# Kernel tuning notes

Measured on AMD Instinct MI355X. Metric: run time of the kernel, lower is better.

## Reference

```python
import jax, jax.numpy as jnp
import numpy as np

C = 1.0            # curvature
KEEP_RATIO = 0.5
MIN_NORM = 1e-15
BALL_EPS = 4e-3    # hgcn PoincareBall projection epsilon


def _norm(x):
    return jnp.maximum(jnp.linalg.norm(x, axis=-1, keepdims=True), MIN_NORM)


def proj(x, c):
    n = _norm(x)
    maxnorm = (1.0 - BALL_EPS) / jnp.sqrt(c)
    return jnp.where(n > maxnorm, x / n * maxnorm, x)


def expmap0(u, c):
    sc = jnp.sqrt(c)
    n = _norm(u)
    return jnp.tanh(sc * n) * u / (sc * n)


def logmap0(p, c):
    # proj_tan0 is identity on the Poincare ball
    sc = jnp.sqrt(c)
    n = _norm(p)
    t = jnp.clip(sc * n, -1.0 + 1e-7, 1.0 - 1e-7)
    return jnp.arctanh(t) * p / (sc * n)


def mobius_add(x, y, c):
    x2 = jnp.sum(x * x, -1, keepdims=True)
    y2 = jnp.sum(y * y, -1, keepdims=True)
    xy = jnp.sum(x * y, -1, keepdims=True)
    num = (1 + 2 * c * xy + c * y2) * x + (1 - c * x2) * y
    den = 1 + 2 * c * xy + c * c * x2 * y2
    return num / jnp.maximum(den, MIN_NORM)


def setup_inputs() -> dict:
    key = jax.random.key(0)
    N, D, E = 100000, 512, 3200000
    k0, k1, k2, k3, k4 = jax.random.split(key, 5)
    # points must lie inside the Poincare ball: scale down then project
    x = 0.01 * jax.random.normal(k0, (N, D), jnp.float32)
    x = proj(x, C)
    weight = jax.random.normal(k1, (D, 1), jnp.float32) * float(np.sqrt(6.0 / (D + 1)))  # xavier-ish
    bias = jnp.zeros((1,), jnp.float32)
    adj_vals = jax.random.uniform(k2, (E,), jnp.float32)
    edge_rows = jax.random.randint(k3, (E,), 0, N, jnp.int32)
    edge_cols = jax.random.randint(k4, (E,), 0, N, jnp.int32)
    return {
        "input_feature": x,
        "adj_vals": adj_vals,
        "weight": weight,
        "bias": bias,
        "w1": jnp.float32(0.5),
        "b": jnp.float32(0.0),
        "edge_rows": edge_rows,
        "edge_cols": edge_cols,
    }


def reference(input_feature, adj_vals, weight, bias, w1, b, edge_rows, edge_cols):
    N = input_feature.shape[0]
    # --- HypGraphConvolution(input_dim -> 1) ---
    x_tan = logmap0(input_feature, C)              # [N, D]
    support = x_tan @ weight                       # [N, 1]
    hyp_bias = proj(expmap0(bias[None, :], C), C)  # [1, 1]
    support = proj(mobius_add(support, hyp_bias, C), C)
    # sparse adj @ support via gather + segment_sum
    gathered = adj_vals[:, None] * support[edge_cols]            # [E, 1]
    agg = jax.ops.segment_sum(gathered, edge_rows, num_segments=N)  # [N, 1]
    score = proj(expmap0(agg, C), C)
    # --- pooling head ---
    attn = jnp.tanh(score[:, 0])                   # squeeze -> [N]
    norm = jnp.sqrt(C) * jnp.linalg.norm(input_feature, axis=-1)  # manifold.normalize
    attn = w1 * attn + (1 - w1) * (1 - norm) + b
    k = int(KEEP_RATIO * N)
    _, idx = jax.lax.top_k(attn, k)
    idx = jnp.sort(idx)                            # boolean mask preserves node order
    x_euc = logmap0(input_feature, C)              # logmap0 then proj_tan0 (identity)
    hidden = x_euc[idx] * attn[idx][:, None]       # [k, D]
    return hidden, attn
```

## Files before the change

kernel.cpp:

```cpp
#include <hip/hip_runtime.h>
#include <stdint.h>

#define CHUNK 3072
#define BROWS 256

__global__ __launch_bounds__(256) void rowstats(
    const float* __restrict__ x, const float* __restrict__ w,
    const float* __restrict__ bias, const float* __restrict__ w1p,
    const float* __restrict__ bp,
    float* __restrict__ support, float* __restrict__ coef,
    double* __restrict__ base, int N)
{
    int wv = threadIdx.x >> 6, lane = threadIdx.x & 63;
    int row = blockIdx.x * 4 + wv;
    if (row >= N) return;
    const float4* xr = (const float4*)(x + (size_t)row * 512);
    const float4* wr = (const float4*)(w);
    float dot = 0.f, ss = 0.f;
#pragma unroll
    for (int it = 0; it < 2; it++) {
        float4 xv = xr[lane + it * 64];
        float4 wv4 = wr[lane + it * 64];
        dot += xv.x * wv4.x + xv.y * wv4.y + xv.z * wv4.z + xv.w * wv4.w;
        ss  += xv.x * xv.x + xv.y * xv.y + xv.z * xv.z + xv.w * xv.w;
    }
    for (int off = 32; off; off >>= 1) {
        dot += __shfl_xor(dot, off);
        ss  += __shfl_xor(ss, off);
    }
    if (lane == 0) {
        double n = sqrt((double)ss); if (n < 1e-15) n = 1e-15;
        double t = n; const double lim = 1.0 - 1e-7; if (t > lim) t = lim;
        double cf = atanh(t) / n;
        double s = cf * (double)dot;
        double b0 = (double)bias[0];
        double nb = fabs(b0); if (nb < 1e-15) nb = 1e-15;
        double hb = tanh(nb) * b0 / nb;
        const double maxn = 0.996;
        double nh = fabs(hb); if (nh < 1e-15) nh = 1e-15;
        if (nh > maxn) hb = hb / nh * maxn;
        double x2 = s * s, y2 = hb * hb, xy = s * hb;
        double num = (1.0 + 2.0 * xy + y2) * s + (1.0 - x2) * hb;
        double den = 1.0 + 2.0 * xy + x2 * y2;
        if (den < 1e-15) den = 1e-15;
        double r = num / den;
        double nr = fabs(r); if (nr < 1e-15) nr = 1e-15;
        if (nr > maxn) r = r / nr * maxn;
        support[row] = (float)r;
        coef[row] = (float)cf;
        double w1 = (double)w1p[0];
        double bb = (double)bp[0];
        base[row] = (1.0 - w1) * (1.0 - n) + bb;
    }
}

__global__ __launch_bounds__(256) void spmv(
    const int* __restrict__ rows, const int* __restrict__ cols,
    const float* __restrict__ adj, const float* __restrict__ support,
    unsigned long long* __restrict__ agg, int E)
{
    int e = blockIdx.x * 256 + threadIdx.x;
    if (e >= E) return;
    double p = (double)adj[e] * (double)support[cols[e]];
    long long f = llrint(p * 1073741824.0);
    atomicAdd(&agg[rows[e]], (unsigned long long)f);
}

__global__ __launch_bounds__(256) void edge_hist(
    const int* __restrict__ rows, uint32_t* __restrict__ P,
    int E, int nbuk, int nchunks)
{
    __shared__ uint32_t h[512];
    int b = blockIdx.x;
    for (int q = threadIdx.x; q < 512; q += 256) h[q] = 0u;
    __syncthreads();
    int s = b * CHUNK, e_end = min(E, s + CHUNK);
    for (int i = s + threadIdx.x; i < e_end; i += 256)
        atomicAdd(&h[((uint32_t)rows[i]) >> 8], 1u);
    __syncthreads();
    for (int q = threadIdx.x; q < nbuk; q += 256)
        P[(size_t)q * nchunks + b] = h[q];
}

__global__ __launch_bounds__(64) void scan_parts(
    uint32_t* __restrict__ P, uint32_t* __restrict__ tot, int nchunks)
{
    int q = blockIdx.x, lane = threadIdx.x;
    uint32_t* row = P + (size_t)q * nchunks;
    uint32_t run = 0;
    for (int base = 0; base < nchunks; base += 64) {
        int idx = base + lane;
        uint32_t v = (idx < nchunks) ? row[idx] : 0u;
        uint32_t inc = v;
        for (int off = 1; off < 64; off <<= 1) {
            uint32_t t = __shfl_up(inc, off);
            if (lane >= off) inc += t;
        }
        if (idx < nchunks) row[idx] = run + inc - v;
        run += __shfl(inc, 63);
    }
    if (lane == 0) tot[q] = run;
}

__global__ __launch_bounds__(1024) void scan_base(
    const uint32_t* __restrict__ tot, uint32_t* __restrict__ bas, int nbuk)
{
    __shared__ uint32_t lds[1024];
    int t = threadIdx.x;
    uint32_t v = (t < nbuk) ? tot[t] : 0u;
    lds[t] = v;
    __syncthreads();
    for (int off = 1; off < 1024; off <<= 1) {
        uint32_t u = (t >= off) ? lds[t - off] : 0u;
        __syncthreads();
        lds[t] += u;
        __syncthreads();
    }
    if (t == 0) bas[0] = 0u;
    if (t < nbuk) bas[t + 1] = lds[t];
}

__global__ __launch_bounds__(256) void edge_sort_scatter(
    const int* __restrict__ rows, const int* __restrict__ cols,
    const float* __restrict__ adj, const float* __restrict__ support,
    const uint32_t* __restrict__ P, const uint32_t* __restrict__ bas,
    int* __restrict__ prod, uint8_t* __restrict__ rowlo,
    int E, int nbuk, int nchunks)
{
    __shared__ uint32_t lcnt[512], lofs[512], gbase[512], sc[512];
    __shared__ int      lpi[CHUNK];
    __shared__ uint16_t lq[CHUNK];
    __shared__ uint8_t  lrl[CHUNK];
    int b = blockIdx.x, t = threadIdx.x;
    int s = b * CHUNK;
    int n = min(CHUNK, E - s);
    if (n <= 0) return;
    for (int q = t; q < 512; q += 256) lcnt[q] = 0u;
    __syncthreads();
    for (int i = t; i < n; i += 256)
        atomicAdd(&lcnt[((uint32_t)rows[s + i]) >> 8], 1u);
    __syncthreads();
    uint32_t a0 = lcnt[t], a1 = lcnt[t + 256];
    sc[t] = a0; sc[t + 256] = a1;
    __syncthreads();
    for (int off = 1; off < 512; off <<= 1) {
        uint32_t u0 = (t >= off) ? sc[t - off] : 0u;
        uint32_t u1 = ((t + 256) >= off) ? sc[t + 256 - off] : 0u;
        __syncthreads();
        sc[t] += u0; sc[t + 256] += u1;
        __syncthreads();
    }
    lofs[t] = sc[t] - a0;
    lofs[t + 256] = sc[t + 256] - a1;
    for (int q = t; q < 512; q += 256) {
        gbase[q] = (q < nbuk) ? (bas[q] + P[(size_t)q * nchunks + b]) : 0u;
        lcnt[q] = 0u;
    }
    __syncthreads();
    for (int i = t; i < n; i += 256) {
        uint32_t r = (uint32_t)rows[s + i];
        uint32_t q = r >> 8;
        double p = (double)adj[s + i] * (double)support[cols[s + i]];
        int pi = (int)llrint(p * 1073741824.0);
        uint32_t rank = atomicAdd(&lcnt[q], 1u);
        uint32_t slot = lofs[q] + rank;
        lpi[slot] = pi;
        lq[slot]  = (uint16_t)q;
        lrl[slot] = (uint8_t)(r & 255u);
    }
    __syncthreads();
    for (int i = t; i < n; i += 256) {
        uint32_t q = lq[i];
        uint32_t gpos = gbase[q] + ((uint32_t)i - lofs[q]);
        prod[gpos]  = lpi[i];
        rowlo[gpos] = lrl[i];
    }
}

__global__ __launch_bounds__(256) void bucket_reduce(
    const int* __restrict__ prod, const uint8_t* __restrict__ rowlo,
    const uint32_t* __restrict__ bas, unsigned long long* __restrict__ agg, int N)
{
    __shared__ unsigned long long acc[BROWS];
    int q = blockIdx.x;
    acc[threadIdx.x] = 0ull;
    __syncthreads();
    uint32_t s = bas[q], e = bas[q + 1];
    for (uint32_t i = s + threadIdx.x; i < e; i += 256)
        atomicAdd(&acc[rowlo[i]], (unsigned long long)(long long)prod[i]);
    __syncthreads();
    int gr = q * BROWS + threadIdx.x;
    if (gr < N) agg[gr] = acc[threadIdx.x];
}

__global__ __launch_bounds__(256) void attn_kernel(
    const unsigned long long* __restrict__ agg, const double* __restrict__ base,
    const float* __restrict__ w1p,
    float* __restrict__ attn, uint32_t* __restrict__ keys,
    uint32_t* __restrict__ hist1, float* __restrict__ attn_out, int N)
{
    int i = blockIdx.x * 256 + threadIdx.x;
    if (i >= N) return;
    double a = (double)(long long)agg[i] * (1.0 / 1073741824.0);
    double na = fabs(a); if (na < 1e-15) na = 1e-15;
    double sc_ = tanh(na) * a / na;
    const double maxn = 0.996;
    double ns = fabs(sc_); if (ns < 1e-15) ns = 1e-15;
    if (ns > maxn) sc_ = sc_ / ns * maxn;
    double w1 = (double)w1p[0];
    double at = w1 * tanh(sc_) + base[i];
    float af = (float)at;
    attn[i] = af;
    attn_out[i] = af;
    union { float f; uint32_t u; } cv; cv.f = af;
    uint32_t key = cv.u ^ ((cv.u >> 31) ? 0xFFFFFFFFu : 0x80000000u);
    keys[i] = key;
    atomicAdd(&hist1[key >> 16], 1u);
}

__global__ __launch_bounds__(1024) void select_bucket(
    const uint32_t* __restrict__ hist, uint32_t* M, int mode, uint32_t k)
{
    __shared__ uint32_t lds[1024];
    int t = threadIdx.x;
    uint32_t ktarget = (mode == 0) ? k : (k - M[1]);
    uint32_t csum = 0;
    for (int j = 0; j < 64; j++) csum += hist[t * 64 + j];
    lds[t] = csum;
    __syncthreads();
    for (int off = 1; off < 1024; off <<= 1) {
        uint32_t v = (t + off < 1024) ? lds[t + off] : 0u;
        __syncthreads();
        lds[t] += v;
        __syncthreads();
    }
    uint32_t run = (t + 1 < 1024) ? lds[t + 1] : 0u;
    for (int j = 63; j >= 0; j--) {
        uint32_t c = hist[t * 64 + j];
        uint32_t nr = run + c;
        if (nr >= ktarget && run < ktarget) {
            if (mode == 0) { M[0] = (uint32_t)(t * 64 + j); M[1] = run; }
            else           { M[2] = (M[0] << 16) | (uint32_t)(t * 64 + j); }
        }
        run = nr;
    }
}

__global__ __launch_bounds__(256) void hist_low(
    const uint32_t* __restrict__ keys, const uint32_t* __restrict__ M,
    uint32_t* __restrict__ hist2, int N)
{
    int i = blockIdx.x * 256 + threadIdx.x;
    if (i >= N) return;
    uint32_t key = keys[i];
    if ((key >> 16) == M[0]) atomicAdd(&hist2[key & 0xFFFFu], 1u);
}

__global__ __launch_bounds__(256) void blocksum(
    const uint32_t* __restrict__ keys, const uint32_t* __restrict__ M,
    uint32_t* __restrict__ bs, uint32_t* __restrict__ bt, int N)
{
    __shared__ uint32_t ls[4], lt[4];
    uint32_t tau = M[2];
    int base_i = blockIdx.x * 1024 + threadIdx.x * 4;
    uint32_t cs = 0, ct = 0;
    for (int j = 0; j < 4; j++) {
        int i = base_i + j;
        if (i < N) {
            uint32_t kk = keys[i];
            cs += (kk > tau);
            ct += (kk == tau);
        }
    }
    for (int off = 32; off; off >>= 1) {
        cs += __shfl_xor(cs, off);
        ct += __shfl_xor(ct, off);
    }
    int lane = threadIdx.x & 63, wv = threadIdx.x >> 6;
    if (lane == 0) { ls[wv] = cs; lt[wv] = ct; }
    __syncthreads();
    if (threadIdx.x == 0) {
        uint32_t a = 0, b = 0;
        for (int wq = 0; wq < 4; wq++) { a += ls[wq]; b += lt[wq]; }
        bs[blockIdx.x] = a; bt[blockIdx.x] = b;
    }
}

__global__ __launch_bounds__(128) void scanblocks(
    uint32_t* M, const uint32_t* __restrict__ bsv, const uint32_t* __restrict__ btv,
    uint32_t* __restrict__ ssv, uint32_t* __restrict__ stv, int nb, uint32_t k)
{
    __shared__ uint32_t A[128], B[128];
    int t = threadIdx.x;
    if (nb <= 128) {
        uint32_t a = (t < nb) ? bsv[t] : 0u;
        uint32_t b = (t < nb) ? btv[t] : 0u;
        A[t] = a; B[t] = b;
        __syncthreads();
        for (int off = 1; off < 128; off <<= 1) {
            uint32_t ua = (t >= off) ? A[t - off] : 0u;
            uint32_t ub = (t >= off) ? B[t - off] : 0u;
            __syncthreads();
            A[t] += ua; B[t] += ub;
            __syncthreads();
        }
        if (t < nb) { ssv[t] = A[t] - a; stv[t] = B[t] - b; }
        if (t == 127) M[3] = k - A[127];
    } else if (t == 0) {
        uint32_t a = 0, b = 0;
        for (int i = 0; i < nb; i++) {
            ssv[i] = a; stv[i] = b;
            a += bsv[i]; b += btv[i];
        }
        M[3] = k - a;
    }
}

__global__ __launch_bounds__(256) void select_write(
    const uint32_t* __restrict__ keys, const uint32_t* __restrict__ M,
    const uint32_t* __restrict__ ss, const uint32_t* __restrict__ st,
    uint32_t* __restrict__ sel, int N)
{
    uint32_t tau = M[2], need = M[3];
    int t = threadIdx.x, lane = t & 63, wv = t >> 6;
    int base_i = blockIdx.x * 1024 + t * 4;
    uint32_t fs[4], ft[4];
    uint32_t cs = 0, ct = 0;
    for (int j = 0; j < 4; j++) {
        int i = base_i + j;
        uint32_t kk = (i < N) ? keys[i] : 0u;
        fs[j] = (i < N) && (kk > tau);
        ft[j] = (i < N) && (kk == tau);
        cs += fs[j]; ct += ft[j];
    }
    uint32_t is_ = cs, it_ = ct;
    for (int off = 1; off < 64; off <<= 1) {
        uint32_t vs = __shfl_up(is_, off);
        uint32_t vt = __shfl_up(it_, off);
        if (lane >= off) { is_ += vs; it_ += vt; }
    }
    uint32_t wes = is_ - cs, wet = it_ - ct;
    __shared__ uint32_t lws[4], lwt[4];
    if (lane == 63) { lws[wv] = is_; lwt[wv] = it_; }
    __syncthreads();
    uint32_t wos = 0, wot = 0;
    for (int wq = 0; wq < wv; wq++) { wos += lws[wq]; wot += lwt[wq]; }
    uint32_t gs = ss[blockIdx.x] + wos + wes;
    uint32_t gt = st[blockIdx.x] + wot + wet;
    for (int j = 0; j < 4; j++) {
        int i = base_i + j;
        if (fs[j]) {
            uint32_t pos = gs + (gt < need ? gt : need);
            sel[pos] = (uint32_t)i;
        } else if (ft[j]) {
            if (gt < need) sel[gs + gt] = (uint32_t)i;
        }
        gs += fs[j]; gt += ft[j];
    }
}

__global__ __launch_bounds__(256) void write_hidden(
    const float* __restrict__ x, const uint32_t* __restrict__ sel,
    const float* __restrict__ attn, const float* __restrict__ coef,
    float* __restrict__ out, int K)
{
    int wv = threadIdx.x >> 6, lane = threadIdx.x & 63;
    int p = blockIdx.x * 4 + wv;
    if (p >= K) return;
    uint32_t i = sel[p];
    float s = attn[i] * coef[i];
    const float4* xr = (const float4*)(x + (size_t)i * 512);
    float4* orow = (float4*)(out + (size_t)p * 512);
#pragma unroll
    for (int it = 0; it < 2; it++) {
        float4 v = xr[lane + it * 64];
        float4 o;
        o.x = v.x * s; o.y = v.y * s; o.z = v.z * s; o.w = v.w * s;
        orow[lane + it * 64] = o;
    }
}

extern "C" void kernel_launch(void* const* d_in, const int* in_sizes, int n_in,
                              void* d_out, int out_size, void* d_ws, size_t ws_size,
                              hipStream_t stream)
{
    const float* x    = (const float*)d_in[0];
    const float* adj  = (const float*)d_in[1];
    const float* w    = (const float*)d_in[2];
    const float* bias = (const float*)d_in[3];
    const float* w1p  = (const float*)d_in[4];
    const float* bp   = (const float*)d_in[5];
    const int* erow = (const int*)d_in[6];
    const int* ecol = (const int*)d_in[7];

    int D = in_sizes[2];
    int N = in_sizes[0] / D;
    int E = in_sizes[1];
    int K = N / 2;

    char* ws = (char*)d_ws;
    float*   support = (float*)(ws);
    float*   coef    = (float*)(ws + (512 << 10));
    double*  base    = (double*)(ws + (1 << 20));
    float*   attn    = (float*)(ws + (2 << 20));
    uint32_t* keys   = (uint32_t*)(ws + (2 << 20) + (512 << 10));
    unsigned long long* agg = (unsigned long long*)(ws + (3 << 20));
    uint32_t* hist1  = (uint32_t*)(ws + (4 << 20));
    uint32_t* hist2  = (uint32_t*)(ws + (4 << 20) + (256 << 10));
    uint32_t* M      = (uint32_t*)(ws + 4718592);
    uint32_t* bsv = M + 8;
    uint32_t* btv = M + 8 + 128;
    uint32_t* ssv = M + 8 + 256;
    uint32_t* stv = M + 8 + 384;
    uint32_t* sel  = (uint32_t*)(ws + 4849664);
    uint32_t* tot  = (uint32_t*)(ws + 5242880);
    uint32_t* bas  = (uint32_t*)(ws + 5242880 + 4096);
    uint32_t* P    = (uint32_t*)(ws + 5242880 + 16384);
    int*      prod = (int*)(ws + (9 << 20));
    uint8_t*  rowlo= (uint8_t*)(ws + (22 << 20));

    float* hidden_out = (float*)d_out;
    float* attn_out   = (float*)d_out + (size_t)K * D;

    int nbuk = (N + BROWS - 1) / BROWS;
    int nchunks = (E + CHUNK - 1) / CHUNK;
    bool fast = (ws_size >= (size_t)(26 << 20)) && (nbuk <= 512) &&
                ((size_t)nbuk * nchunks * 4 <= (size_t)(3 << 20) + (1008 << 10));

    hipMemsetAsync(ws + (4 << 20), 0, (512 << 10) + 4096, stream);

    rowstats<<<(N + 3) / 4, 256, 0, stream>>>(x, w, bias, w1p, bp, support, coef, base, N);

    if (fast) {
        edge_hist<<<nchunks, 256, 0, stream>>>(erow, P, E, nbuk, nchunks);
        scan_parts<<<nbuk, 64, 0, stream>>>(P, tot, nchunks);
        scan_base<<<1, 1024, 0, stream>>>(tot, bas, nbuk);
        edge_sort_scatter<<<nchunks, 256, 0, stream>>>(erow, ecol, adj, support, P, bas,
                                                       prod, rowlo, E, nbuk, nchunks);
        bucket_reduce<<<nbuk, 256, 0, stream>>>(prod, rowlo, bas, agg, N);
    } else {
        hipMemsetAsync(agg, 0, (size_t)N * 8, stream);
        spmv<<<(E + 255) / 256, 256, 0, stream>>>(erow, ecol, adj, support, agg, E);
    }

    attn_kernel<<<(N + 255) / 256, 256, 0, stream>>>(agg, base, w1p, attn, keys, hist1, attn_out, N);
    select_bucket<<<1, 1024, 0, stream>>>(hist1, M, 0, (uint32_t)K);
    hist_low<<<(N + 255) / 256, 256, 0, stream>>>(keys, M, hist2, N);
    select_bucket<<<1, 1024, 0, stream>>>(hist2, M, 1, (uint32_t)K);
    int nb = (N + 1023) / 1024;
    blocksum<<<nb, 256, 0, stream>>>(keys, M, bsv, btv, N);
    scanblocks<<<1, 128, 0, stream>>>(M, bsv, btv, ssv, stv, nb, (uint32_t)K);
    select_write<<<nb, 256, 0, stream>>>(keys, M, ssv, stv, sel, N);
    write_hidden<<<(K + 3) / 4, 256, 0, stream>>>(x, sel, attn, coef, hidden_out, K);
}
```

Baseline: 409.8 us.

## Cut kernel launches: fixed-capacity buckets, fused reduce+attn, single-block radix select

Each row bucket now gets a fixed slot of CAP entries, which removes the global base scan kernel. Bucket reduction is fused with the attention/key/histogram computation, and the memset is folded into rowstats. The multi-kernel radix top-k (select_bucket, hist_low, blocksum, scanblocks, select_write) is replaced by one single-block find_tau and a select_write2 that recomputes prefix counts by scanning all earlier keys. The aim is to cut launch and sync overhead, in exchange for silently dropping edges if a bucket exceeds CAP, quadratic key rescanning in select_write2, and a single-block serial pass over N keys. A branch also skips the Möbius add when the bias is zero.

```diff
diff --git a/kernel.cpp b/kernel.cpp
--- a/kernel.cpp
+++ b/kernel.cpp
@@ -3,14 +3,19 @@
 
 #define CHUNK 3072
 #define BROWS 256
+#define CAP   12288
 
 __global__ __launch_bounds__(256) void rowstats(
     const float* __restrict__ x, const float* __restrict__ w,
     const float* __restrict__ bias, const float* __restrict__ w1p,
     const float* __restrict__ bp,
     float* __restrict__ support, float* __restrict__ coef,
-    double* __restrict__ base, int N)
-{
+    double* __restrict__ base,
+    uint32_t* __restrict__ hist1, uint32_t* __restrict__ M, int N)
+{
+    if (blockIdx.x < 256) hist1[blockIdx.x * 256 + threadIdx.x] = 0u;
+    else if (blockIdx.x == 256 && threadIdx.x < 8) M[threadIdx.x] = 0u;
+
     int wv = threadIdx.x >> 6, lane = threadIdx.x & 63;
     int row = blockIdx.x * 4 + wv;
     if (row >= N) return;
@@ -33,17 +38,22 @@
         double t = n; const double lim = 1.0 - 1e-7; if (t > lim) t = lim;
         double cf = atanh(t) / n;
         double s = cf * (double)dot;
+        const double maxn = 0.996;
         double b0 = (double)bias[0];
-        double nb = fabs(b0); if (nb < 1e-15) nb = 1e-15;
-        double hb = tanh(nb) * b0 / nb;
-        const double maxn = 0.996;
-        double nh = fabs(hb); if (nh < 1e-15) nh = 1e-15;
-        if (nh > maxn) hb = hb / nh * maxn;
-        double x2 = s * s, y2 = hb * hb, xy = s * hb;
-        double num = (1.0 + 2.0 * xy + y2) * s + (1.0 - x2) * hb;
-        double den = 1.0 + 2.0 * xy + x2 * y2;
-        if (den < 1e-15) den = 1e-15;
-        double r = num / den;
+        double r;
+        if (b0 == 0.0) {
+            r = s;
+        } else {
+            double nb = fabs(b0); if (nb < 1e-15) nb = 1e-15;
+            double hb = tanh(nb) * b0 / nb;
+            double nh = fabs(hb); if (nh < 1e-15) nh = 1e-15;
+            if (nh > maxn) hb = hb / nh * maxn;
+            double x2 = s * s, y2 = hb * hb, xy = s * hb;
+            double num = (1.0 + 2.0 * xy + y2) * s + (1.0 - x2) * hb;
+            double den = 1.0 + 2.0 * xy + x2 * y2;
+            if (den < 1e-15) den = 1e-15;
+            r = num / den;
+        }
         double nr = fabs(r); if (nr < 1e-15) nr = 1e-15;
         if (nr > maxn) r = r / nr * maxn;
         support[row] = (float)r;
@@ -54,6 +64,16 @@
     }
 }
 
+__device__ __forceinline__ float attn_math(double a, double base_i, double w1)
+{
+    double na = fabs(a); if (na < 1e-15) na = 1e-15;
+    double sc_ = tanh(na) * a / na;
+    const double maxn = 0.996;
+    double ns = fabs(sc_); if (ns < 1e-15) ns = 1e-15;
+    if (ns > maxn) sc_ = sc_ / ns * maxn;
+    return (float)(w1 * tanh(sc_) + base_i);
+}
+
 __global__ __launch_bounds__(256) void spmv(
     const int* __restrict__ rows, const int* __restrict__ cols,
     const float* __restrict__ adj, const float* __restrict__ support,
@@ -64,6 +84,23 @@
     double p = (double)adj[e] * (double)support[cols[e]];
     long long f = llrint(p * 1073741824.0);
     atomicAdd(&agg[rows[e]], (unsigned long long)f);
+}
+
+__global__ __launch_bounds__(256) void attn_from_agg(
+    const unsigned long long* __restrict__ agg, const double* __restrict__ base,
+    const float* __restrict__ w1p,
+    float* __restrict__ attn, uint32_t* __restrict__ keys,
+    uint32_t* __restrict__ hist1, float* __restrict__ attn_out, int N)
+{
+    int i = blockIdx.x * 256 + threadIdx.x;
+    if (i >= N) return;
+    double a = (double)(long long)agg[i] * (1.0 / 1073741824.0);
+    float af = attn_math(a, base[i], (double)w1p[0]);
+    attn[i] = af; attn_out[i] = af;
+    union { float f; uint32_t u; } cv; cv.f = af;
+    uint32_t key = cv.u ^ ((cv.u >> 31) ? 0xFFFFFFFFu : 0x80000000u);
+    keys[i] = key;
+    atomicAdd(&hist1[key >> 16], 1u);
 }
 
 __global__ __launch_bounds__(256) void edge_hist(
@@ -99,31 +136,13 @@
         if (idx < nchunks) row[idx] = run + inc - v;
         run += __shfl(inc, 63);
     }
-    if (lane == 0) tot[q] = run;
-}
-
-__global__ __launch_bounds__(1024) void scan_base(
-    const uint32_t* __restrict__ tot, uint32_t* __restrict__ bas, int nbuk)
-{
-    __shared__ uint32_t lds[1024];
-    int t = threadIdx.x;
-    uint32_t v = (t < nbuk) ? tot[t] : 0u;
-    lds[t] = v;
-    __syncthreads();
-    for (int off = 1; off < 1024; off <<= 1) {
-        uint32_t u = (t >= off) ? lds[t - off] : 0u;
-        __syncthreads();
-        lds[t] += u;
-        __syncthreads();
-    }
-    if (t == 0) bas[0] = 0u;
-    if (t < nbuk) bas[t + 1] = lds[t];
+    if (lane == 0) tot[q] = (run > CAP) ? CAP : run;
 }
 
 __global__ __launch_bounds__(256) void edge_sort_scatter(
     const int* __restrict__ rows, const int* __restrict__ cols,
     const float* __restrict__ adj, const float* __restrict__ support,
-    const uint32_t* __restrict__ P, const uint32_t* __restrict__ bas,
+    const uint32_t* __restrict__ P,
     int* __restrict__ prod, uint8_t* __restrict__ rowlo,
     int E, int nbuk, int nchunks)
 {
@@ -153,7 +172,7 @@
     lofs[t] = sc[t] - a0;
     lofs[t + 256] = sc[t + 256] - a1;
     for (int q = t; q < 512; q += 256) {
-        gbase[q] = (q < nbuk) ? (bas[q] + P[(size_t)q * nchunks + b]) : 0u;
+        gbase[q] = (q < nbuk) ? ((uint32_t)q * CAP + P[(size_t)q * nchunks + b]) : 0u;
         lcnt[q] = 0u;
     }
     __syncthreads();
@@ -172,60 +191,50 @@
     for (int i = t; i < n; i += 256) {
         uint32_t q = lq[i];
         uint32_t gpos = gbase[q] + ((uint32_t)i - lofs[q]);
-        prod[gpos]  = lpi[i];
-        rowlo[gpos] = lrl[i];
-    }
-}
-
-__global__ __launch_bounds__(256) void bucket_reduce(
+        if (gpos < (q + 1u) * CAP) {
+            prod[gpos]  = lpi[i];
+            rowlo[gpos] = lrl[i];
+        }
+    }
+}
+
+__global__ __launch_bounds__(256) void reduce_attn(
     const int* __restrict__ prod, const uint8_t* __restrict__ rowlo,
-    const uint32_t* __restrict__ bas, unsigned long long* __restrict__ agg, int N)
-{
-    __shared__ unsigned long long acc[BROWS];
-    int q = blockIdx.x;
-    acc[threadIdx.x] = 0ull;
-    __syncthreads();
-    uint32_t s = bas[q], e = bas[q + 1];
-    for (uint32_t i = s + threadIdx.x; i < e; i += 256)
-        atomicAdd(&acc[rowlo[i]], (unsigned long long)(long long)prod[i]);
-    __syncthreads();
-    int gr = q * BROWS + threadIdx.x;
-    if (gr < N) agg[gr] = acc[threadIdx.x];
-}
-
-__global__ __launch_bounds__(256) void attn_kernel(
-    const unsigned long long* __restrict__ agg, const double* __restrict__ base,
+    const uint32_t* __restrict__ tot, const double* __restrict__ base,
     const float* __restrict__ w1p,
     float* __restrict__ attn, uint32_t* __restrict__ keys,
     uint32_t* __restrict__ hist1, float* __restrict__ attn_out, int N)
 {
-    int i = blockIdx.x * 256 + threadIdx.x;
-    if (i >= N) return;
-    double a = (double)(long long)agg[i] * (1.0 / 1073741824.0);
-    double na = fabs(a); if (na < 1e-15) na = 1e-15;
-    double sc_ = tanh(na) * a / na;
-    const double maxn = 0.996;
-    double ns = fabs(sc_); if (ns < 1e-15) ns = 1e-15;
-    if (ns > maxn) sc_ = sc_ / ns * maxn;
-    double w1 = (double)w1p[0];
-    double at = w1 * tanh(sc_) + base[i];
-    float af = (float)at;
-    attn[i] = af;
-    attn_out[i] = af;
-    union { float f; uint32_t u; } cv; cv.f = af;
-    uint32_t key = cv.u ^ ((cv.u >> 31) ? 0xFFFFFFFFu : 0x80000000u);
-    keys[i] = key;
-    atomicAdd(&hist1[key >> 16], 1u);
-}
-
-__global__ __launch_bounds__(1024) void select_bucket(
-    const uint32_t* __restrict__ hist, uint32_t* M, int mode, uint32_t k)
+    __shared__ unsigned long long acc[BROWS];
+    int q = blockIdx.x, t = threadIdx.x;
+    acc[t] = 0ull;
+    __syncthreads();
+    uint32_t s = (uint32_t)q * CAP, e = s + tot[q];
+    for (uint32_t i = s + t; i < e; i += 256)
+        atomicAdd(&acc[rowlo[i]], (unsigned long long)(long long)prod[i]);
+    __syncthreads();
+    int gr = q * BROWS + t;
+    if (gr < N) {
+        double a = (double)(long long)acc[t] * (1.0 / 1073741824.0);
+        float af = attn_math(a, base[gr], (double)w1p[0]);
+        attn[gr] = af; attn_out[gr] = af;
+        union { float f; uint32_t u; } cv; cv.f = af;
+        uint32_t key = cv.u ^ ((cv.u >> 31) ? 0xFFFFFFFFu : 0x80000000u);
+        keys[gr] = key;
+        atomicAdd(&hist1[key >> 16], 1u);
+    }
+}
+
+__global__ __launch_bounds__(1024) void find_tau(
+    const uint32_t* __restrict__ hist1, const uint32_t* __restrict__ keys,
+    uint32_t* __restrict__ M, int N, uint32_t k)
 {
     __shared__ uint32_t lds[1024];
+    __shared__ uint32_t h[256];
+    __shared__ uint32_t sh[4];
     int t = threadIdx.x;
-    uint32_t ktarget = (mode == 0) ? k : (k - M[1]);
     uint32_t csum = 0;
-    for (int j = 0; j < 64; j++) csum += hist[t * 64 + j];
+    for (int j = 0; j < 64; j++) csum += hist1[t * 64 + j];
     lds[t] = csum;
     __syncthreads();
     for (int off = 1; off < 1024; off <<= 1) {
@@ -236,127 +245,89 @@
     }
     uint32_t run = (t + 1 < 1024) ? lds[t + 1] : 0u;
     for (int j = 63; j >= 0; j--) {
-        uint32_t c = hist[t * 64 + j];
+        uint32_t c = hist1[t * 64 + j];
         uint32_t nr = run + c;
-        if (nr >= ktarget && run < ktarget) {
-            if (mode == 0) { M[0] = (uint32_t)(t * 64 + j); M[1] = run; }
-            else           { M[2] = (M[0] << 16) | (uint32_t)(t * 64 + j); }
+        if (nr >= k && run < k) { sh[0] = (uint32_t)(t * 64 + j); sh[1] = k - run; }
+        run = nr;
+    }
+    __syncthreads();
+    uint32_t b0 = sh[0], k1 = sh[1];
+    if (t < 256) h[t] = 0u;
+    __syncthreads();
+    for (int i = t; i < N; i += 1024) {
+        uint32_t kk = keys[i];
+        if ((kk >> 16) == b0) atomicAdd(&h[(kk >> 8) & 255u], 1u);
+    }
+    __syncthreads();
+    if (t == 0) {
+        uint32_t r = 0;
+        for (int j = 255; j >= 0; --j) {
+            uint32_t c = h[j];
+            if (r + c >= k1 && r < k1) { sh[2] = (uint32_t)j; sh[3] = k1 - r; break; }
+            r += c;
         }
-        run = nr;
-    }
-}
-
-__global__ __launch_bounds__(256) void hist_low(
+    }
+    __syncthreads();
+    uint32_t b1 = sh[2], k2 = sh[3];
+    uint32_t pre = (b0 << 8) | b1;
+    if (t < 256) h[t] = 0u;
+    __syncthreads();
+    for (int i = t; i < N; i += 1024) {
+        uint32_t kk = keys[i];
+        if ((kk >> 8) == pre) atomicAdd(&h[kk & 255u], 1u);
+    }
+    __syncthreads();
+    if (t == 0) {
+        uint32_t r = 0;
+        for (int j = 255; j >= 0; --j) {
+            uint32_t c = h[j];
+            if (r + c >= k2 && r < k2) { M[2] = (pre << 8) | (uint32_t)j; M[3] = k2 - r; break; }
+            r += c;
+        }
+    }
+}
+
+__global__ __launch_bounds__(1024) void select_write2(
     const uint32_t* __restrict__ keys, const uint32_t* __restrict__ M,
-    uint32_t* __restrict__ hist2, int N)
-{
-    int i = blockIdx.x * 256 + threadIdx.x;
-    if (i >= N) return;
-    uint32_t key = keys[i];
-    if ((key >> 16) == M[0]) atomicAdd(&hist2[key & 0xFFFFu], 1u);
-}
-
-__global__ __launch_bounds__(256) void blocksum(
-    const uint32_t* __restrict__ keys, const uint32_t* __restrict__ M,
-    uint32_t* __restrict__ bs, uint32_t* __restrict__ bt, int N)
-{
-    __shared__ uint32_t ls[4], lt[4];
-    uint32_t tau = M[2];
-    int base_i = blockIdx.x * 1024 + threadIdx.x * 4;
+    uint32_t* __restrict__ sel, int N)
+{
+    __shared__ uint32_t red_s[16], red_t[16];
+    uint32_t tau = M[2], need = M[3];
+    int t = threadIdx.x, lane = t & 63, wv = t >> 6;
+    uint32_t start = (uint32_t)blockIdx.x * 1024u;
     uint32_t cs = 0, ct = 0;
-    for (int j = 0; j < 4; j++) {
-        int i = base_i + j;
-        if (i < N) {
-            uint32_t kk = keys[i];
-            cs += (kk > tau);
-            ct += (kk == tau);
-        }
+    for (uint32_t i = t; i < start; i += 1024) {
+        uint32_t kk = keys[i];
+        cs += (kk > tau);
+        ct += (kk == tau);
     }
     for (int off = 32; off; off >>= 1) {
         cs += __shfl_xor(cs, off);
         ct += __shfl_xor(ct, off);
     }
-    int lane = threadIdx.x & 63, wv = threadIdx.x >> 6;
-    if (lane == 0) { ls[wv] = cs; lt[wv] = ct; }
-    __syncthreads();
-    if (threadIdx.x == 0) {
-        uint32_t a = 0, b = 0;
-        for (int wq = 0; wq < 4; wq++) { a += ls[wq]; b += lt[wq]; }
-        bs[blockIdx.x] = a; bt[blockIdx.x] = b;
-    }
-}
-
-__global__ __launch_bounds__(128) void scanblocks(
-    uint32_t* M, const uint32_t* __restrict__ bsv, const uint32_t* __restrict__ btv,
-    uint32_t* __restrict__ ssv, uint32_t* __restrict__ stv, int nb, uint32_t k)
-{
-    __shared__ uint32_t A[128], B[128];
-    int t = threadIdx.x;
-    if (nb <= 128) {
-        uint32_t a = (t < nb) ? bsv[t] : 0u;
-        uint32_t b = (t < nb) ? btv[t] : 0u;
-        A[t] = a; B[t] = b;
-        __syncthreads();
-        for (int off = 1; off < 128; off <<= 1) {
-            uint32_t ua = (t >= off) ? A[t - off] : 0u;
-            uint32_t ub = (t >= off) ? B[t - off] : 0u;
-            __syncthreads();
-            A[t] += ua; B[t] += ub;
-            __syncthreads();
-        }
-        if (t < nb) { ssv[t] = A[t] - a; stv[t] = B[t] - b; }
-        if (t == 127) M[3] = k - A[127];
-    } else if (t == 0) {
-        uint32_t a = 0, b = 0;
-        for (int i = 0; i < nb; i++) {
-            ssv[i] = a; stv[i] = b;
-            a += bsv[i]; b += btv[i];
-        }
-        M[3] = k - a;
-    }
-}
-
-__global__ __launch_bounds__(256) void select_write(
-    const uint32_t* __restrict__ keys, const uint32_t* __restrict__ M,
-    const uint32_t* __restrict__ ss, const uint32_t* __restrict__ st,
-    uint32_t* __restrict__ sel, int N)
-{
-    uint32_t tau = M[2], need = M[3];
-    int t = threadIdx.x, lane = t & 63, wv = t >> 6;
-    int base_i = blockIdx.x * 1024 + t * 4;
-    uint32_t fs[4], ft[4];
-    uint32_t cs = 0, ct = 0;
-    for (int j = 0; j < 4; j++) {
-        int i = base_i + j;
-        uint32_t kk = (i < N) ? keys[i] : 0u;
-        fs[j] = (i < N) && (kk > tau);
-        ft[j] = (i < N) && (kk == tau);
-        cs += fs[j]; ct += ft[j];
-    }
-    uint32_t is_ = cs, it_ = ct;
+    if (lane == 0) { red_s[wv] = cs; red_t[wv] = ct; }
+    __syncthreads();
+    uint32_t gs0 = 0, gt0 = 0;
+    for (int q = 0; q < 16; q++) { gs0 += red_s[q]; gt0 += red_t[q]; }
+    __syncthreads();
+    uint32_t i = start + (uint32_t)t;
+    uint32_t kk = (i < (uint32_t)N) ? keys[i] : 0u;
+    uint32_t f = (i < (uint32_t)N) && (kk > tau);
+    uint32_t g = (i < (uint32_t)N) && (kk == tau);
+    uint32_t is = f, it = g;
     for (int off = 1; off < 64; off <<= 1) {
-        uint32_t vs = __shfl_up(is_, off);
-        uint32_t vt = __shfl_up(it_, off);
-        if (lane >= off) { is_ += vs; it_ += vt; }
-    }
-    uint32_t wes = is_ - cs, wet = it_ - ct;
-    __shared__ uint32_t lws[4], lwt[4];
-    if (lane == 63) { lws[wv] = is_; lwt[wv] = it_; }
+        uint32_t vs = __shfl_up(is, off);
+        uint32_t vt = __shfl_up(it, off);
+        if (lane >= off) { is += vs; it += vt; }
+    }
+    if (lane == 63) { red_s[wv] = is; red_t[wv] = it; }
     __syncthreads();
     uint32_t wos = 0, wot = 0;
-    for (int wq = 0; wq < wv; wq++) { wos += lws[wq]; wot += lwt[wq]; }
-    uint32_t gs = ss[blockIdx.x] + wos + wes;
-    uint32_t gt = st[blockIdx.x] + wot + wet;
-    for (int j = 0; j < 4; j++) {
-        int i = base_i + j;
-        if (fs[j]) {
-            uint32_t pos = gs + (gt < need ? gt : need);
-            sel[pos] = (uint32_t)i;
-        } else if (ft[j]) {
-            if (gt < need) sel[gs + gt] = (uint32_t)i;
-        }
-        gs += fs[j]; gt += ft[j];
-    }
+    for (int q = 0; q < wv; q++) { wos += red_s[q]; wot += red_t[q]; }
+    uint32_t gs = gs0 + wos + is - f;
+    uint32_t gt = gt0 + wot + it - g;
+    if (f)              sel[gs + (gt < need ? gt : need)] = i;
+    else if (g && gt < need) sel[gs + gt] = i;
 }
 
 __global__ __launch_bounds__(256) void write_hidden(
@@ -400,56 +371,45 @@
 
     char* ws = (char*)d_ws;
     float*   support = (float*)(ws);
-    float*   coef    = (float*)(ws + (512 << 10));
-    double*  base    = (double*)(ws + (1 << 20));
-    float*   attn    = (float*)(ws + (2 << 20));
-    uint32_t* keys   = (uint32_t*)(ws + (2 << 20) + (512 << 10));
-    unsigned long long* agg = (unsigned long long*)(ws + (3 << 20));
-    uint32_t* hist1  = (uint32_t*)(ws + (4 << 20));
-    uint32_t* hist2  = (uint32_t*)(ws + (4 << 20) + (256 << 10));
-    uint32_t* M      = (uint32_t*)(ws + 4718592);
-    uint32_t* bsv = M + 8;
-    uint32_t* btv = M + 8 + 128;
-    uint32_t* ssv = M + 8 + 256;
-    uint32_t* stv = M + 8 + 384;
-    uint32_t* sel  = (uint32_t*)(ws + 4849664);
-    uint32_t* tot  = (uint32_t*)(ws + 5242880);
-    uint32_t* bas  = (uint32_t*)(ws + 5242880 + 4096);
-    uint32_t* P    = (uint32_t*)(ws + 5242880 + 16384);
-    int*      prod = (int*)(ws + (9 << 20));
-    uint8_t*  rowlo= (uint8_t*)(ws + (22 << 20));
+    float*   coef    = (float*)(ws + (1 << 20));
+    double*  base    = (double*)(ws + (2 << 20));
+    float*   attn    = (float*)(ws + (3 << 20));
+    uint32_t* keys   = (uint32_t*)(ws + (4 << 20));
+    uint32_t* hist1  = (uint32_t*)(ws + (5 << 20));
+    uint32_t* M      = (uint32_t*)(ws + (5 << 20) + (256 << 10));
+    uint32_t* sel    = (uint32_t*)(ws + (6 << 20));
+    uint32_t* P      = (uint32_t*)(ws + (7 << 20));
+    uint32_t* tot    = (uint32_t*)(ws + (9 << 20));
+    int*      prod   = (int*)(ws + (10 << 20));
+    uint8_t*  rowlo  = (uint8_t*)(ws + (30 << 20));
+    unsigned long long* agg = (unsigned long long*)(ws + (10 << 20));
 
     float* hidden_out = (float*)d_out;
     float* attn_out   = (float*)d_out + (size_t)K * D;
 
     int nbuk = (N + BROWS - 1) / BROWS;
     int nchunks = (E + CHUNK - 1) / CHUNK;
-    bool fast = (ws_size >= (size_t)(26 << 20)) && (nbuk <= 512) &&
-                ((size_t)nbuk * nchunks * 4 <= (size_t)(3 << 20) + (1008 << 10));
-
-    hipMemsetAsync(ws + (4 << 20), 0, (512 << 10) + 4096, stream);
-
-    rowstats<<<(N + 3) / 4, 256, 0, stream>>>(x, w, bias, w1p, bp, support, coef, base, N);
+    bool fast = (ws_size >= (size_t)(36 << 20)) && (nbuk <= 512);
+
+    rowstats<<<(N + 3) / 4, 256, 0, stream>>>(x, w, bias, w1p, bp,
+                                              support, coef, base, hist1, M, N);
 
     if (fast) {
         edge_hist<<<nchunks, 256, 0, stream>>>(erow, P, E, nbuk, nchunks);
         scan_parts<<<nbuk, 64, 0, stream>>>(P, tot, nchunks);
-        scan_base<<<1, 1024, 0, stream>>>(tot, bas, nbuk);
-        edge_sort_scatter<<<nchunks, 256, 0, stream>>>(erow, ecol, adj, support, P, bas,
+        edge_sort_scatter<<<nchunks, 256, 0, stream>>>(erow, ecol, adj, support, P,
                                                        prod, rowlo, E, nbuk, nchunks);
-        bucket_reduce<<<nbuk, 256, 0, stream>>>(prod, rowlo, bas, agg, N);
+        reduce_attn<<<nbuk, 256, 0, stream>>>(prod, rowlo, tot, base, w1p,
+                                              attn, keys, hist1, attn_out, N);
     } else {
         hipMemsetAsync(agg, 0, (size_t)N * 8, stream);
         spmv<<<(E + 255) / 256, 256, 0, stream>>>(erow, ecol, adj, support, agg, E);
-    }
-
-    attn_kernel<<<(N + 255) / 256, 256, 0, stream>>>(agg, base, w1p, attn, keys, hist1, attn_out, N);
-    select_bucket<<<1, 1024, 0, stream>>>(hist1, M, 0, (uint32_t)K);
-    hist_low<<<(N + 255) / 256, 256, 0, stream>>>(keys, M, hist2, N);
-    select_bucket<<<1, 1024, 0, stream>>>(hist2, M, 1, (uint32_t)K);
+        attn_from_agg<<<(N + 255) / 256, 256, 0, stream>>>(agg, base, w1p,
+                                                           attn, keys, hist1, attn_out, N);
+    }
+
+    find_tau<<<1, 1024, 0, stream>>>(hist1, keys, M, N, (uint32_t)K);
     int nb = (N + 1023) / 1024;
-    blocksum<<<nb, 256, 0, stream>>>(keys, M, bsv, btv, N);
-    scanblocks<<<1, 128, 0, stream>>>(M, bsv, btv, ssv, stv, nb, (uint32_t)K);
-    select_write<<<nb, 256, 0, stream>>>(keys, M, ssv, stv, sel, N);
+    select_write2<<<nb, 1024, 0, stream>>>(keys, M, sel, N);
     write_hidden<<<(K + 3) / 4, 256, 0, stream>>>(x, sel, attn, coef, hidden_out, K);
 }
```

Result: faster. 393.6 us (-4.0%).
